# Performance work log

Hardware: AMD Instinct MI355X
Metric: run time of the kernel (lower is better)

The kernel has to match this reference:

```python
import jax, jax.numpy as jnp
import numpy as np

NUM_HEADS = 12
AGENT_NUM = 49

def setup_inputs() -> dict:
    key = jax.random.key(0)
    ks = jax.random.split(key, 5)
    B, N, C = 32, 1176, 768
    x = jax.random.normal(ks[0], (B, N, C), dtype=jnp.float32)
    qkv_w = jax.random.normal(ks[1], (3 * C, C), dtype=jnp.float32) * 0.02
    qkv_b = jax.random.normal(ks[2], (3 * C,), dtype=jnp.float32) * 0.02
    proj_w = jax.random.normal(ks[3], (C, C), dtype=jnp.float32) * 0.02
    proj_b = jax.random.normal(ks[4], (C,), dtype=jnp.float32) * 0.02
    return {"x": x, "qkv_w": qkv_w, "qkv_b": qkv_b, "proj_w": proj_w,
            "proj_b": proj_b, "t_h": 14, "t_w": 14, "s_h": 28, "s_w": 28}

def _softmax_clamped(a):
    # original: float32 clamp to finfo min/max, then softmax(dim=-1)
    fi = jnp.finfo(jnp.float32)
    a = jnp.clip(a.astype(jnp.float32), fi.min, fi.max)
    return jax.nn.softmax(a, axis=-1)

def reference(x, qkv_w, qkv_b, proj_w, proj_b, t_h, t_w, s_h, s_w):
    B, N, C = x.shape
    H = NUM_HEADS
    hd = C // H
    scale = hd ** -0.5
    n_mt = 2 * t_h * t_w
    n_s = s_h * s_w

    qkv = (x @ qkv_w.T + qkv_b).reshape(B, N, 3, H, hd).transpose(2, 0, 3, 1, 4)
    q, k, v = qkv[0], qkv[1], qkv[2]  # [B,H,N,hd]

    q_mt, q_s = q[:, :, :n_mt], q[:, :, n_mt:]
    k_mt = k[:, :, :n_mt]
    v_mt = v[:, :, :n_mt]

    # stage 1: template/memory self-attention
    attn = _softmax_clamped(jnp.einsum('bhqd,bhkd->bhqk', q_mt, k_mt) * scale)
    x_mt = jnp.einsum('bhqk,bhkd->bhqd', attn, v_mt).transpose(0, 2, 1, 3).reshape(B, n_mt, C)

    # agent tokens: pool q_s (replicates original layout-scrambling reshape)
    p = int(AGENT_NUM ** 0.5)  # 7
    agent = q_s.reshape(B, s_h, s_w, C).transpose(0, 3, 1, 2)  # [B,C,s_h,s_w]
    agent = agent.reshape(B, C, p, s_h // p, p, s_w // p).mean(axis=(3, 5))  # exact AdaptiveAvgPool2d(7,7)
    agent = agent.reshape(B, C, AGENT_NUM).transpose(0, 2, 1)  # [B,agent_num,C]
    agent = agent.reshape(B, AGENT_NUM, H, hd).transpose(0, 2, 1, 3)  # [B,H,agent_num,hd]

    # stage 2: agent attends to all keys
    agent_attn = _softmax_clamped(jnp.einsum('bhad,bhkd->bhak', agent * scale, k))
    agent_v = jnp.einsum('bhak,bhkd->bhad', agent_attn, v)  # [B,H,agent_num,hd]

    # stage 3: search queries attend to agent tokens
    q_attn = _softmax_clamped(jnp.einsum('bhqd,bhad->bhqa', q_s * scale, agent))
    x_s = jnp.einsum('bhqa,bhad->bhqd', q_attn, agent_v).transpose(0, 2, 1, 3).reshape(B, n_s, C)

    out = jnp.concatenate([x_mt, x_s], axis=1)
    out = out @ proj_w.T + proj_b
    return out
```

## Files before the change

kernel.cpp:

```cpp
#include <hip/hip_runtime.h>

typedef __attribute__((ext_vector_type(8))) short short8;
typedef __attribute__((ext_vector_type(4))) short short4v;
typedef __attribute__((ext_vector_type(4))) float f32x4;
typedef unsigned short u16;

#define B_    32
#define N_    1176
#define C_    768
#define H_    12
#define HD_   64
#define NMT_  392
#define AG_   49
#define NEGBIG_ (-1.0e4f)

__device__ __forceinline__ u16 f2bf(float f) {
  unsigned u = __float_as_uint(f);
  unsigned r = (u + 0x7fffu + ((u >> 16) & 1u)) >> 16;
  return (u16)r;
}
__device__ __forceinline__ float bf2f(u16 s) {
  return __uint_as_float(((unsigned)s) << 16);
}

__device__ __forceinline__ int xcd_swz(int g, int nwg) {
  const int q = nwg >> 3, r = nwg & 7;
  const int xcd = g & 7, off = g >> 3;
  return (xcd < r ? xcd * (q + 1) : r * (q + 1) + (xcd - r) * q) + off;
}

__global__ __launch_bounds__(256) void split_all(
    const float* __restrict__ x, u16* __restrict__ xbf, int n4x,
    const float* __restrict__ qw, u16* __restrict__ qwh, int n4q,
    const float* __restrict__ pw, u16* __restrict__ pwh,
    u16* __restrict__ pwl, int n4p) {
  const int bid = blockIdx.x;
  const float* in;
  u16 *hi, *lo = nullptr;
  int n4, i0, nblk;
  if (bid < 2048) {
    in = x; hi = xbf; n4 = n4x; i0 = bid; nblk = 2048;
  } else if (bid < 3072) {
    in = qw; hi = qwh; n4 = n4q; i0 = bid - 2048; nblk = 1024;
  } else {
    in = pw; hi = pwh; lo = pwl; n4 = n4p; i0 = bid - 3072; nblk = 512;
  }
  int i = i0 * 256 + threadIdx.x;
  const int stride = nblk * 256;
  const bool dolo = (lo != nullptr);
  for (; i < n4; i += stride) {
    const float4 v = ((const float4*)in)[i];
    const float f[4] = {v.x, v.y, v.z, v.w};
    short4v h, l;
#pragma unroll
    for (int e = 0; e < 4; ++e) {
      u16 hb = f2bf(f[e]);
      h[e] = (short)hb;
      l[e] = (short)f2bf(f[e] - bf2f(hb));
    }
    ((short4v*)hi)[i] = h;
    if (dolo) ((short4v*)lo)[i] = l;
  }
}

__global__ __launch_bounds__(256, 3) void gemm_qkv(
    const u16* __restrict__ A, const u16* __restrict__ Bw,
    const float* __restrict__ bias, u16* __restrict__ qb, u16* __restrict__ kb,
    u16* __restrict__ vb, int Mch) {
  __shared__ u16 SH[17408];
  u16* As = SH;
  u16* Bs = SH + 8192;
  const int tid = threadIdx.x;
  const int swz = xcd_swz(blockIdx.x, gridDim.x);
  const int half = gridDim.x >> 1;
  const int cg = swz / half;
  const int rem = swz - cg * half;
  const int brow = rem / 9;
  const int bcol = cg * 9 + (rem - brow * 9);
  const int m0 = brow * 128, c0 = bcol * 128;
  const int lane = tid & 63, w = tid >> 6;
  const int wr = w >> 1, wc = w & 1;
  const int fr = lane & 15, ko = lane >> 4;
  const int lsw = (lane * 8) ^ (ko << 4);

  f32x4 acc[4][4];
#pragma unroll
  for (int m = 0; m < 4; ++m)
#pragma unroll
    for (int n = 0; n < 4; ++n) acc[m][n] = (f32x4)0.f;

  short8 ra[4], rb[4];
  auto LOADG = [&](int kt) {
#pragma unroll
    for (int i = 0; i < 4; ++i) {
      const int ch = tid + i * 256;
      const int row = ch >> 3, slotk = ch & 7;
      const int ar = min(m0 + row, Mch - 1);
      ra[i] = *(const short8*)&A[(size_t)ar * 768 + kt * 64 + slotk * 8];
      rb[i] = *(const short8*)&Bw[(size_t)(c0 + row) * 768 + kt * 64 + slotk * 8];
    }
  };
  auto WRITE = [&]() {
#pragma unroll
    for (int i = 0; i < 4; ++i) {
      const int ch = tid + i * 256;
      const int row = ch >> 3, slotk = ch & 7;
      const int s = slotk >> 2, sl = slotk & 3;
      const int off = (row >> 4) * 1024 + s * 512 +
                      ((sl * 128 + (row & 15) * 8) ^ (sl << 4));
      *(short8*)&As[off] = ra[i];
      *(short8*)&Bs[off] = rb[i];
    }
  };

  LOADG(0);
  for (int kt = 0; kt < 12; ++kt) {
    __syncthreads();
    WRITE();
    if (kt < 11) LOADG(kt + 1);
    __syncthreads();
#pragma unroll
    for (int s = 0; s < 2; ++s) {
      short8 af[4], bfr[4];
#pragma unroll
      for (int m = 0; m < 4; ++m)
        af[m] = *(const short8*)&As[((wr * 4 + m) * 2 + s) * 512 + lsw];
#pragma unroll
      for (int n = 0; n < 4; ++n)
        bfr[n] = *(const short8*)&Bs[((wc * 4 + n) * 2 + s) * 512 + lsw];
#pragma unroll
      for (int m = 0; m < 4; ++m)
#pragma unroll
        for (int n = 0; n < 4; ++n)
          acc[m][n] = __builtin_amdgcn_mfma_f32_16x16x32_bf16(af[m], bfr[n], acc[m][n], 0, 0, 0);
    }
  }

  __syncthreads();
  const int t = c0 / 768;
  const int hbase = (c0 % 768) >> 6;
  if (t < 2) {
#pragma unroll
    for (int n = 0; n < 4; ++n) {
      const int col = wc * 64 + n * 16 + fr;
      const float bv = bias[c0 + col];
#pragma unroll
      for (int m = 0; m < 4; ++m)
#pragma unroll
        for (int r = 0; r < 4; ++r) {
          const int row = wr * 64 + m * 16 + ko * 4 + r;
          SH[row * 136 + col] = f2bf(acc[m][n][r] + bv);
        }
    }
    __syncthreads();
    u16* dst = (t == 0) ? qb : kb;
    for (int it = tid; it < 2048; it += 256) {
      const int rt = it >> 4, half2 = (it >> 3) & 1, p = it & 7;
      const int mg = m0 + rt;
      if (mg < Mch) {
        const int bl = mg / N_, nt = mg - bl * N_;
        const short8 vv = *(const short8*)&SH[rt * 136 + half2 * 64 + p * 8];
        *(short8*)&dst[(((size_t)bl * H_ + hbase + half2) * N_ + nt) * 64 + p * 8] = vv;
      }
    }
  } else {
#pragma unroll
    for (int n = 0; n < 4; ++n) {
      const int col = wc * 64 + n * 16 + fr;
      const float bv = bias[c0 + col];
#pragma unroll
      for (int m = 0; m < 4; ++m)
#pragma unroll
        for (int r = 0; r < 4; ++r) {
          const int row = wr * 64 + m * 16 + ko * 4 + r;
          SH[col * 136 + row] = f2bf(acc[m][n][r] + bv);
        }
    }
    __syncthreads();
    for (int it = tid; it < 2048; it += 256) {
      const int ct = it >> 4, tc = it & 15;
      const int mg0 = m0 + tc * 8;
      if (mg0 < Mch) {
        const int bl = mg0 / N_, nt = mg0 - bl * N_;
        const int d = ct & 63, hh = hbase + (ct >> 6);
        const short8 vv = *(const short8*)&SH[ct * 136 + tc * 8];
        *(short8*)&vb[(((size_t)bl * H_ + hh) * 64 + d) * N_ + nt] = vv;
      }
    }
  }
}

__global__ __launch_bounds__(256, 3) void gemm_proj(
    const u16* __restrict__ Ahg, const u16* __restrict__ Bhg,
    const u16* __restrict__ Blg, const float* __restrict__ bias,
    float* __restrict__ out) {
  __shared__ u16 Ah[8192], Bh[8192], Bl[8192];
  const int tid = threadIdx.x;
  const int swz = xcd_swz(blockIdx.x, gridDim.x);
  const int brow = swz / 6, bcol = swz - brow * 6;
  const int m0 = brow * 128, c0 = bcol * 128;
  const int lane = tid & 63, w = tid >> 6;
  const int wr = w >> 1, wc = w & 1;
  const int fr = lane & 15, ko = lane >> 4;
  const int lsw = (lane * 8) ^ (ko << 4);

  f32x4 acc[4][4];
#pragma unroll
  for (int m = 0; m < 4; ++m)
#pragma unroll
    for (int n = 0; n < 4; ++n) acc[m][n] = (f32x4)0.f;

  short8 rah[4], rbh[4], rbl[4];
  auto LOADG = [&](int kt) {
#pragma unroll
    for (int i = 0; i < 4; ++i) {
      const int ch = tid + i * 256;
      const int row = ch >> 3, slotk = ch & 7;
      const size_t aoff = (size_t)(m0 + row) * 768 + kt * 64 + slotk * 8;
      const size_t boff = (size_t)(c0 + row) * 768 + kt * 64 + slotk * 8;
      rah[i] = *(const short8*)&Ahg[aoff];
      rbh[i] = *(const short8*)&Bhg[boff];
      rbl[i] = *(const short8*)&Blg[boff];
    }
  };
  auto WRITE = [&]() {
#pragma unroll
    for (int i = 0; i < 4; ++i) {
      const int ch = tid + i * 256;
      const int row = ch >> 3, slotk = ch & 7;
      const int s = slotk >> 2, sl = slotk & 3;
      const int off = (row >> 4) * 1024 + s * 512 +
                      ((sl * 128 + (row & 15) * 8) ^ (sl << 4));
      *(short8*)&Ah[off] = rah[i];
      *(short8*)&Bh[off] = rbh[i];
      *(short8*)&Bl[off] = rbl[i];
    }
  };

  LOADG(0);
  for (int kt = 0; kt < 12; ++kt) {
    __syncthreads();
    WRITE();
    if (kt < 11) LOADG(kt + 1);
    __syncthreads();
#pragma unroll
    for (int s = 0; s < 2; ++s) {
      short8 ah[4], bh[4], bl[4];
#pragma unroll
      for (int m = 0; m < 4; ++m)
        ah[m] = *(const short8*)&Ah[((wr * 4 + m) * 2 + s) * 512 + lsw];
#pragma unroll
      for (int n = 0; n < 4; ++n) {
        const int off = ((wc * 4 + n) * 2 + s) * 512 + lsw;
        bh[n] = *(const short8*)&Bh[off];
        bl[n] = *(const short8*)&Bl[off];
      }
#pragma unroll
      for (int m = 0; m < 4; ++m)
#pragma unroll
        for (int n = 0; n < 4; ++n) {
          acc[m][n] = __builtin_amdgcn_mfma_f32_16x16x32_bf16(ah[m], bh[n], acc[m][n], 0, 0, 0);
          acc[m][n] = __builtin_amdgcn_mfma_f32_16x16x32_bf16(ah[m], bl[n], acc[m][n], 0, 0, 0);
        }
    }
  }
#pragma unroll
  for (int n = 0; n < 4; ++n) {
    const int col = c0 + wc * 64 + n * 16 + fr;
    const float bv = bias[col];
#pragma unroll
    for (int m = 0; m < 4; ++m) {
      const int mg = m0 + wr * 64 + m * 16 + ko * 4;
#pragma unroll
      for (int r = 0; r < 4; ++r) out[(size_t)(mg + r) * 768 + col] = acc[m][n][r] + bv;
    }
  }
}

__global__ __launch_bounds__(256) void agent_pool(const u16* __restrict__ q,
                                                  u16* __restrict__ agent) {
  const int wid = threadIdx.x >> 6;
  const int lane = threadIdx.x & 63;
  const int row = blockIdx.x * 4 + wid;
  const int rem = row % (H_ * 64);
  const int b = row / (H_ * 64);
  const int h2 = rem / 64;
  const int a = rem % 64;
  if (a >= AG_) {
    agent[((size_t)b * H_ + h2) * 4096 + a * 64 + lane] = 0;
    return;
  }
  const int ap = a / 7, aq = a % 7;
  float s = 0.f;
#pragma unroll
  for (int i = 0; i < 4; ++i)
#pragma unroll
    for (int j = 0; j < 4; ++j) {
      const int g = (ap * 4 + i) * 336 + (aq * 4 + j) * 12 + h2;
      const int h = g / 784, n = g % 784;
      s += bf2f(q[(((size_t)b * H_ + h) * N_ + NMT_ + n) * HD_ + lane]);
    }
  agent[((size_t)b * H_ + h2) * 4096 + a * 64 + lane] = f2bf(s * 0.0625f);
}

__global__ __launch_bounds__(256, 3) void flash_attn(
    const u16* __restrict__ Q, int q_bh_str, int q_base, int q_row_max, int q_valid,
    const u16* __restrict__ K, int k_bh_str, int k_row_max,
    const u16* __restrict__ Vt, int vt_bh_str, int vt_pitch, int vt_col_max,
    int n_keys, int nkt,
    u16* __restrict__ cch, int b0,
    u16* __restrict__ avT, int mode) {
  __shared__ u16 Qs[4096], Ks[4096], Vts[4096], Ps[4096];
  __shared__ float Ss[64][68];
  __shared__ float mS[64], lS[64], aS[64];

  const int tid = threadIdx.x, bh = blockIdx.x;
  const int q0 = q_base + blockIdx.y * 56;
  const int lane = tid & 63, w = tid >> 6;
  const int fr = lane & 15, ko = lane >> 4;

  const u16* Qb = Q + (size_t)bh * q_bh_str;
  const u16* Kb = K + (size_t)bh * k_bh_str;
  const u16* Vb = Vt + (size_t)bh * vt_bh_str;

#pragma unroll
  for (int i = 0; i < 2; ++i) {
    const int ch = tid + i * 256;
    const int row = ch >> 3, c8 = (ch & 7) << 3;
    const int qr = min(q0 + row, q_row_max);
    const short8 v = *(const short8*)&Qb[(size_t)qr * 64 + c8];
    *(short8*)&Qs[(row * 64 + c8) ^ ((row & 7) << 3)] = v;
  }
  if (tid < 64) { mS[tid] = NEGBIG_; lS[tid] = 0.f; aS[tid] = 0.f; }

  f32x4 oacc[4];
#pragma unroll
  for (int d = 0; d < 4; ++d) oacc[d] = (f32x4)0.f;

  for (int kt = 0; kt < nkt; ++kt) {
#pragma unroll
    for (int i = 0; i < 2; ++i) {
      const int ch = tid + i * 256;
      const int row = ch >> 3, c8 = (ch & 7) << 3;
      const int kr = min(kt * 64 + row, k_row_max);
      const short8 v = *(const short8*)&Kb[(size_t)kr * 64 + c8];
      *(short8*)&Ks[(row * 64 + c8) ^ ((row & 7) << 3)] = v;
    }
#pragma unroll
    for (int i = 0; i < 2; ++i) {
      const int ch = tid + i * 256;
      const int row = ch >> 3, c8 = (ch & 7) << 3;
      const int col8 = kt * 64 + c8;
      const u16* src = &Vb[(size_t)row * vt_pitch];
      short8 v;
      if (col8 + 8 <= vt_col_max) {
        v = *(const short8*)&src[col8];
      } else {
#pragma unroll
        for (int e = 0; e < 8; ++e) v[e] = (short)src[min(col8 + e, vt_col_max - 1)];
      }
      *(short8*)&Vts[(row * 64 + c8) ^ ((row & 7) << 3)] = v;
    }
    __syncthreads();

    short8 aq[2];
#pragma unroll
    for (int s = 0; s < 2; ++s)
      aq[s] = *(const short8*)&Qs[((w * 16 + fr) * 64 + s * 32 + ko * 8) ^ ((fr & 7) << 3)];
#pragma unroll
    for (int j = 0; j < 4; ++j) {
      f32x4 sa = (f32x4)0.f;
#pragma unroll
      for (int s = 0; s < 2; ++s) {
        const short8 bk = *(const short8*)&Ks[((j * 16 + fr) * 64 + s * 32 + ko * 8) ^ ((fr & 7) << 3)];
        sa = __builtin_amdgcn_mfma_f32_16x16x32_bf16(aq[s], bk, sa, 0, 0, 0);
      }
      const int colg = kt * 64 + j * 16 + fr;
      const bool maskc = (colg >= n_keys);
#pragma unroll
      for (int r = 0; r < 4; ++r) {
        const int srow = w * 16 + ko * 4 + r;
        Ss[srow][j * 16 + fr] = maskc ? NEGBIG_ : sa[r] * 0.125f;
      }
    }
    __syncthreads();

    {
      const int r = tid >> 2, jj = tid & 3;
      float sv[16];
      float mx = NEGBIG_;
#pragma unroll
      for (int cc = 0; cc < 4; ++cc) {
        const f32x4 v4 = *(const f32x4*)&Ss[r][jj * 16 + cc * 4];
#pragma unroll
        for (int e = 0; e < 4; ++e) {
          sv[cc * 4 + e] = v4[e];
          mx = fmaxf(mx, v4[e]);
        }
      }
      mx = fmaxf(mx, __shfl_xor(mx, 1));
      mx = fmaxf(mx, __shfl_xor(mx, 2));
      const float mold = mS[r];
      const float mnew = fmaxf(mold, mx);
      float sum = 0.f;
      const int pbase = r * 64 + jj * 16;
      const int px = (r & 7) << 3;
#pragma unroll
      for (int hh = 0; hh < 2; ++hh) {
        short8 ph;
#pragma unroll
        for (int c = 0; c < 8; ++c) {
          const bool mk = (kt * 64 + jj * 16 + hh * 8 + c) >= n_keys;
          const float p = mk ? 0.f : __expf(sv[hh * 8 + c] - mnew);
          sum += p;
          ph[c] = (short)f2bf(p);
        }
        *(short8*)&Ps[(pbase + hh * 8) ^ px] = ph;
      }
      sum += __shfl_xor(sum, 1);
      sum += __shfl_xor(sum, 2);
      if (jj == 0) {
        const float alpha = __expf(mold - mnew);
        aS[r] = alpha;
        lS[r] = lS[r] * alpha + sum;
        mS[r] = mnew;
      }
    }
    __syncthreads();

    float al[4];
#pragma unroll
    for (int r = 0; r < 4; ++r) al[r] = aS[w * 16 + ko * 4 + r];
    short8 ap[2];
#pragma unroll
    for (int s = 0; s < 2; ++s)
      ap[s] = *(const short8*)&Ps[((w * 16 + fr) * 64 + s * 32 + ko * 8) ^ ((fr & 7) << 3)];
#pragma unroll
    for (int dj = 0; dj < 4; ++dj) {
      f32x4 o = oacc[dj];
#pragma unroll
      for (int r = 0; r < 4; ++r) o[r] *= al[r];
#pragma unroll
      for (int s = 0; s < 2; ++s) {
        const short8 bv = *(const short8*)&Vts[((dj * 16 + fr) * 64 + s * 32 + ko * 8) ^ ((fr & 7) << 3)];
        o = __builtin_amdgcn_mfma_f32_16x16x32_bf16(ap[s], bv, o, 0, 0, 0);
      }
      oacc[dj] = o;
    }
    __syncthreads();
  }

  float linv[4];
#pragma unroll
  for (int r = 0; r < 4; ++r) linv[r] = 1.f / fmaxf(lS[w * 16 + ko * 4 + r], 1e-30f);

  if (mode == 0) {
    const int b = bh / H_, h = bh % H_;
#pragma unroll
    for (int dj = 0; dj < 4; ++dj)
#pragma unroll
      for (int r = 0; r < 4; ++r) {
        const int rowl = w * 16 + ko * 4 + r;
        if (rowl < q_valid) {
          const size_t m = (size_t)(b0 + b) * N_ + q0 + rowl;
          cch[m * 768 + h * 64 + dj * 16 + fr] = f2bf(oacc[dj][r] * linv[r]);
        }
      }
  } else {
#pragma unroll
    for (int dj = 0; dj < 4; ++dj)
#pragma unroll
      for (int r = 0; r < 4; ++r) {
        const int a = w * 16 + ko * 4 + r;
        avT[(size_t)bh * 4096 + (dj * 16 + fr) * 64 + a] = f2bf(oacc[dj][r] * linv[r]);
      }
  }
}

extern "C" void kernel_launch(void* const* d_in, const int* in_sizes, int n_in,
                              void* d_out, int out_size, void* d_ws,
                              size_t ws_size, hipStream_t stream) {
  const float* x = (const float*)d_in[0];
  const float* qkv_w = (const float*)d_in[1];
  const float* qkv_b = (const float*)d_in[2];
  const float* proj_w = (const float*)d_in[3];
  const float* proj_b = (const float*)d_in[4];
  float* out = (float*)d_out;
  u16* ws = (u16*)d_ws;

  const size_t XBF = 28901376ull;
  const size_t QW = 2304ull * 768;
  const size_t PW = 768ull * 768;
  const size_t QKV1 = (size_t)H_ * N_ * HD_;
  const size_t AG1 = (size_t)H_ * 64 * 64;

  size_t o = 0;
  u16* xbf = ws + o; o += XBF;
  u16* qwh = ws + o; o += QW;
  u16* pwh = ws + o; o += PW;
  u16* pwl = ws + o; o += PW;
  u16* cch = ws + o; o += XBF;
  const size_t fixed_sh = o;
  const size_t per_sh = 3 * QKV1 + 2 * AG1;

  int cb = 1;
  const int cands[6] = {32, 16, 8, 4, 2, 1};
  for (int i = 0; i < 6; ++i)
    if ((fixed_sh + (size_t)cands[i] * per_sh) * 2 <= ws_size) { cb = cands[i]; break; }

  u16* qb = ws + o; o += cb * QKV1;
  u16* kb = ws + o; o += cb * QKV1;
  u16* vb = ws + o; o += cb * QKV1;
  u16* agent = ws + o; o += cb * AG1;
  u16* avT = ws + o; o += cb * AG1;

  split_all<<<3584, 256, 0, stream>>>(x, xbf, (int)(XBF / 4),
                                      qkv_w, qwh, (int)(QW / 4),
                                      proj_w, pwh, pwl, (int)(PW / 4));

  const int nch = B_ / cb;
  for (int chn = 0; chn < nch; ++chn) {
    const int b0 = chn * cb;
    const int Mch = cb * N_;
    const int nrow = (Mch + 127) / 128;
    gemm_qkv<<<dim3(nrow * 18), 256, 0, stream>>>(
        xbf + (size_t)b0 * N_ * 768, qwh, qkv_b, qb, kb, vb, Mch);
    agent_pool<<<dim3(cb * 192), 256, 0, stream>>>(qb, agent);
    flash_attn<<<dim3(cb * H_, 1), 256, 0, stream>>>(
        agent, 4096, 0, 48, AG_, kb, N_ * HD_, N_ - 1,
        vb, N_ * HD_, N_, N_, N_, 19, nullptr, b0, avT, 1);
    flash_attn<<<dim3(cb * H_, 7), 256, 0, stream>>>(
        qb, N_ * HD_, 0, N_ - 1, 56, kb, N_ * HD_, N_ - 1,
        vb, N_ * HD_, N_, N_, NMT_, 7, cch, b0, nullptr, 0);
    flash_attn<<<dim3(cb * H_, 14), 256, 0, stream>>>(
        qb, N_ * HD_, NMT_, N_ - 1, 56, agent, 4096, 63,
        avT, 4096, 64, 64, AG_, 1, cch, b0, nullptr, 0);
  }
  gemm_proj<<<dim3(294 * 6), 256, 0, stream>>>(cch, pwh, pwl, proj_b, out);
}
```

Before: 519.4 us.

## Enlarge QKV GEMM tile to 256 rows with 512-thread blocks

The QKV projection GEMM now uses 512-thread blocks computing 256x128 output tiles instead of 256x128-thread 128x128 tiles. The B (weight) tile is shared by twice as many rows, which halves weight reloads per output, and the grid shrinks accordingly. The epilogue is split into two passes that stage half the tile at a time through shared memory. The cost is more shared memory per block, fewer resident blocks, a tighter register budget under the new launch bounds, and an extra epilogue barrier round.

Result: no change. 509.5 us (-1.9%).

```diff
diff --git a/kernel.cpp b/kernel.cpp
--- a/kernel.cpp
+++ b/kernel.cpp
@@ -63,13 +63,13 @@
   }
 }
 
-__global__ __launch_bounds__(256, 3) void gemm_qkv(
+__global__ __launch_bounds__(512, 4) void gemm_qkv(
     const u16* __restrict__ A, const u16* __restrict__ Bw,
     const float* __restrict__ bias, u16* __restrict__ qb, u16* __restrict__ kb,
     u16* __restrict__ vb, int Mch) {
-  __shared__ u16 SH[17408];
+  __shared__ u16 SH[24576];
   u16* As = SH;
-  u16* Bs = SH + 8192;
+  u16* Bs = SH + 16384;
   const int tid = threadIdx.x;
   const int swz = xcd_swz(blockIdx.x, gridDim.x);
   const int half = gridDim.x >> 1;
@@ -77,7 +77,7 @@
   const int rem = swz - cg * half;
   const int brow = rem / 9;
   const int bcol = cg * 9 + (rem - brow * 9);
-  const int m0 = brow * 128, c0 = bcol * 128;
+  const int m0 = brow * 256, c0 = bcol * 128;
   const int lane = tid & 63, w = tid >> 6;
   const int wr = w >> 1, wc = w & 1;
   const int fr = lane & 15, ko = lane >> 4;
@@ -89,26 +89,39 @@
 #pragma unroll
     for (int n = 0; n < 4; ++n) acc[m][n] = (f32x4)0.f;
 
-  short8 ra[4], rb[4];
+  short8 ra[4], rb[2];
   auto LOADG = [&](int kt) {
 #pragma unroll
     for (int i = 0; i < 4; ++i) {
-      const int ch = tid + i * 256;
+      const int ch = tid + i * 512;
       const int row = ch >> 3, slotk = ch & 7;
       const int ar = min(m0 + row, Mch - 1);
       ra[i] = *(const short8*)&A[(size_t)ar * 768 + kt * 64 + slotk * 8];
+    }
+#pragma unroll
+    for (int i = 0; i < 2; ++i) {
+      const int ch = tid + i * 512;
+      const int row = ch >> 3, slotk = ch & 7;
       rb[i] = *(const short8*)&Bw[(size_t)(c0 + row) * 768 + kt * 64 + slotk * 8];
     }
   };
   auto WRITE = [&]() {
 #pragma unroll
     for (int i = 0; i < 4; ++i) {
-      const int ch = tid + i * 256;
+      const int ch = tid + i * 512;
       const int row = ch >> 3, slotk = ch & 7;
       const int s = slotk >> 2, sl = slotk & 3;
       const int off = (row >> 4) * 1024 + s * 512 +
                       ((sl * 128 + (row & 15) * 8) ^ (sl << 4));
       *(short8*)&As[off] = ra[i];
+    }
+#pragma unroll
+    for (int i = 0; i < 2; ++i) {
+      const int ch = tid + i * 512;
+      const int row = ch >> 3, slotk = ch & 7;
+      const int s = slotk >> 2, sl = slotk & 3;
+      const int off = (row >> 4) * 1024 + s * 512 +
+                      ((sl * 128 + (row & 15) * 8) ^ (sl << 4));
       *(short8*)&Bs[off] = rb[i];
     }
   };
@@ -136,55 +149,67 @@
     }
   }
 
-  __syncthreads();
   const int t = c0 / 768;
   const int hbase = (c0 % 768) >> 6;
-  if (t < 2) {
-#pragma unroll
-    for (int n = 0; n < 4; ++n) {
-      const int col = wc * 64 + n * 16 + fr;
-      const float bv = bias[c0 + col];
-#pragma unroll
-      for (int m = 0; m < 4; ++m)
-#pragma unroll
-        for (int r = 0; r < 4; ++r) {
-          const int row = wr * 64 + m * 16 + ko * 4 + r;
-          SH[row * 136 + col] = f2bf(acc[m][n][r] + bv);
-        }
-    }
-    __syncthreads();
-    u16* dst = (t == 0) ? qb : kb;
-    for (int it = tid; it < 2048; it += 256) {
-      const int rt = it >> 4, half2 = (it >> 3) & 1, p = it & 7;
-      const int mg = m0 + rt;
-      if (mg < Mch) {
-        const int bl = mg / N_, nt = mg - bl * N_;
-        const short8 vv = *(const short8*)&SH[rt * 136 + half2 * 64 + p * 8];
-        *(short8*)&dst[(((size_t)bl * H_ + hbase + half2) * N_ + nt) * 64 + p * 8] = vv;
-      }
-    }
-  } else {
-#pragma unroll
-    for (int n = 0; n < 4; ++n) {
-      const int col = wc * 64 + n * 16 + fr;
-      const float bv = bias[c0 + col];
-#pragma unroll
-      for (int m = 0; m < 4; ++m)
-#pragma unroll
-        for (int r = 0; r < 4; ++r) {
-          const int row = wr * 64 + m * 16 + ko * 4 + r;
-          SH[col * 136 + row] = f2bf(acc[m][n][r] + bv);
-        }
-    }
-    __syncthreads();
-    for (int it = tid; it < 2048; it += 256) {
-      const int ct = it >> 4, tc = it & 15;
-      const int mg0 = m0 + tc * 8;
-      if (mg0 < Mch) {
-        const int bl = mg0 / N_, nt = mg0 - bl * N_;
-        const int d = ct & 63, hh = hbase + (ct >> 6);
-        const short8 vv = *(const short8*)&SH[ct * 136 + tc * 8];
-        *(short8*)&vb[(((size_t)bl * H_ + hh) * 64 + d) * N_ + nt] = vv;
+#pragma unroll
+  for (int p2 = 0; p2 < 2; ++p2) {
+    __syncthreads();
+    if ((wr >> 1) == p2) {
+      const int lbase = (wr & 1) * 64;
+      if (t < 2) {
+#pragma unroll
+        for (int n = 0; n < 4; ++n) {
+          const int col = wc * 64 + n * 16 + fr;
+          const float bv = bias[c0 + col];
+#pragma unroll
+          for (int m = 0; m < 4; ++m)
+#pragma unroll
+            for (int r = 0; r < 4; ++r) {
+              const int lrow = lbase + m * 16 + ko * 4 + r;
+              SH[lrow * 136 + col] = f2bf(acc[m][n][r] + bv);
+            }
+        }
+      } else {
+#pragma unroll
+        for (int n = 0; n < 4; ++n) {
+          const int col = wc * 64 + n * 16 + fr;
+          const float bv = bias[c0 + col];
+#pragma unroll
+          for (int m = 0; m < 4; ++m)
+#pragma unroll
+            for (int r = 0; r < 4; ++r) {
+              const int lrow = lbase + m * 16 + ko * 4 + r;
+              SH[col * 136 + lrow] = f2bf(acc[m][n][r] + bv);
+            }
+        }
+      }
+    }
+    __syncthreads();
+    if (t < 2) {
+      u16* dst = (t == 0) ? qb : kb;
+#pragma unroll
+      for (int it = 0; it < 4; ++it) {
+        const int idx = tid + it * 512;
+        const int rt = idx >> 4, half2 = (idx >> 3) & 1, p = idx & 7;
+        const int mg = m0 + p2 * 128 + rt;
+        if (mg < Mch) {
+          const int bl = mg / N_, nt = mg - bl * N_;
+          const short8 vv = *(const short8*)&SH[rt * 136 + half2 * 64 + p * 8];
+          *(short8*)&dst[(((size_t)bl * H_ + hbase + half2) * N_ + nt) * 64 + p * 8] = vv;
+        }
+      }
+    } else {
+#pragma unroll
+      for (int it = 0; it < 4; ++it) {
+        const int idx = tid + it * 512;
+        const int ct = idx >> 4, tc = idx & 15;
+        const int mg0 = m0 + p2 * 128 + tc * 8;
+        if (mg0 < Mch) {
+          const int bl = mg0 / N_, nt = mg0 - bl * N_;
+          const int d = ct & 63, hh = hbase + (ct >> 6);
+          const short8 vv = *(const short8*)&SH[ct * 136 + tc * 8];
+          *(short8*)&vb[(((size_t)bl * H_ + hh) * 64 + d) * N_ + nt] = vv;
+        }
       }
     }
   }
@@ -522,8 +547,8 @@
   for (int chn = 0; chn < nch; ++chn) {
     const int b0 = chn * cb;
     const int Mch = cb * N_;
-    const int nrow = (Mch + 127) / 128;
-    gemm_qkv<<<dim3(nrow * 18), 256, 0, stream>>>(
+    const int nrow = (Mch + 255) / 256;
+    gemm_qkv<<<dim3(nrow * 18), 512, 0, stream>>>(
         xbf + (size_t)b0 * N_ * 768, qwh, qkv_b, qb, kb, vb, Mch);
     agent_pool<<<dim3(cb * 192), 256, 0, stream>>>(qb, agent);
     flash_attn<<<dim3(cb * H_, 1), 256, 0, stream>>>(
```
